# Optimization experiments

Measured on AMD Instinct MI355X. Metric: run time of the kernel, lower is better.

## Reference

```python
import jax, jax.numpy as jnp
import numpy as np

B, Q, D = 4, 1024, 1024
N, DH = 16, 64  # n_head, d_head
SCALE = 1.0 / DH ** 0.5
LN_EPS = 1e-5


def setup_inputs() -> dict:
    key = jax.random.key(0)
    ks = jax.random.split(key, 10)
    return {
        "w": jax.random.normal(ks[0], (B, Q, D), jnp.float32),
        "r_emb": jax.random.normal(ks[1], (Q, N, DH), jnp.float32),
        "r_w_bias": jax.random.normal(ks[2], (N, DH), jnp.float32),
        "r_bias": jax.random.normal(ks[3], (Q, N), jnp.float32),
        # projection weights stored [in, out]; torch Linear init std = 1/sqrt(d_head)
        "Wq": jax.random.normal(ks[4], (D, N * DH), jnp.float32) * SCALE,
        "Wk": jax.random.normal(ks[5], (D, N * DH), jnp.float32) * SCALE,
        "Wv": jax.random.normal(ks[6], (D, N * DH), jnp.float32) * SCALE,
        "Wo": jax.random.normal(ks[7], (N * DH, D), jnp.float32) * SCALE,
        "ln_gamma": jnp.ones((D,), jnp.float32),
        "ln_beta": jnp.zeros((D,), jnp.float32),
    }


def _rel_shift(x):
    # x: [b, i, j, n]; pad a zero column at the end of j then drop j=0
    # equivalent to shifting left by one along j with a trailing zero.
    return jnp.concatenate([x[:, :, 1:, :], jnp.zeros_like(x[:, :, :1, :])], axis=2)


def reference(w, r_emb, r_w_bias, r_bias, Wq, Wk, Wv, Wo, ln_gamma, ln_beta):
    b, qlen, d = w.shape
    klen = qlen  # mems=None
    n, dh = r_w_bias.shape

    q_h = (w @ Wq).reshape(b, qlen, n, dh)
    k_h = (w @ Wk).reshape(b, klen, n, dh)
    v_h = (w @ Wv).reshape(b, klen, n, dh)

    rw_q = q_h + r_w_bias[None, None]                      # [b,q,n,dh]
    AC = jnp.einsum('bind,bjnd->bijn', rw_q, k_h)          # [b,q,k,n]
    B_ = jnp.einsum('bind,jnd->bijn', q_h, r_emb)          # [b,q,k,n]
    BD = _rel_shift(B_ + r_bias[None, None])               # [b,q,k,n]

    attn_score = (AC + BD) * SCALE
    attn_prob = jax.nn.softmax(attn_score, axis=2)
    attn_vec = jnp.einsum('bijn,bjnd->bind', attn_prob, v_h)
    attn_out = attn_vec.reshape(b, qlen, n * dh) @ Wo

    out = w + attn_out  # residual (post-lnorm path)
    mu = jnp.mean(out, axis=-1, keepdims=True)
    var = jnp.var(out, axis=-1, keepdims=True)
    return (out - mu) / jnp.sqrt(var + LN_EPS) * ln_gamma + ln_beta
```

## Files before the change

### kernel.cpp

```cpp
#include <hip/hip_runtime.h>
#include <hip/hip_bf16.h>

using f16 = _Float16;
typedef _Float16 f16x8 __attribute__((ext_vector_type(8)));
typedef _Float16 f16x4 __attribute__((ext_vector_type(4)));
typedef float f32x4 __attribute__((ext_vector_type(4)));

#define AS1 __attribute__((address_space(1)))
#define AS3 __attribute__((address_space(3)))

constexpr int Bc = 4, Qc = 1024, Dc = 1024, Nh = 16, DHc = 64;
constexpr int BQ = Bc * Qc;
constexpr int NHEAD = Bc * Nh;
constexpr float ATT_SCALE = 0.125f;

__global__ void k_f2h(const float* __restrict__ src, f16* __restrict__ dst) {
    long i8 = ((long)blockIdx.x * blockDim.x + threadIdx.x) * 8;
    float4 a = *(const float4*)&src[i8];
    float4 b = *(const float4*)&src[i8 + 4];
    f16x8 o = { (f16)a.x, (f16)a.y, (f16)a.z, (f16)a.w,
                (f16)b.x, (f16)b.y, (f16)b.z, (f16)b.w };
    *(f16x8*)&dst[i8] = o;
}

struct Ptr4 { const float* p[4]; };
__global__ void k_transpose4(Ptr4 srcs, f16* __restrict__ dst) {
    __shared__ f16 tile[32][33];
    const float* src = srcs.p[blockIdx.z];
    f16* d = dst + (long)blockIdx.z * Dc * Dc;
    int c0 = blockIdx.x * 32, r0 = blockIdx.y * 32;
#pragma unroll
    for (int dy = 0; dy < 32; dy += 8) {
        int r = r0 + threadIdx.y + dy, c = c0 + threadIdx.x;
        tile[threadIdx.y + dy][threadIdx.x] = (f16)src[(long)r * Dc + c];
    }
    __syncthreads();
#pragma unroll
    for (int dy = 0; dy < 32; dy += 8) {
        int c = c0 + threadIdx.y + dy, r = r0 + threadIdx.x;
        d[(long)c * Dc + r] = tile[threadIdx.x][threadIdx.y + dy];
    }
}

__global__ void k_fill_remb(const float* __restrict__ remb, f16* __restrict__ Kt) {
    long gid = (long)blockIdx.x * blockDim.x + threadIdx.x;
    int d8 = (int)(gid & 7) * 8;
    int j = (int)((gid >> 3) & 1023);
    int h = (int)(gid >> 13);
    int n = h & 15;
    f16x8 kv;
    if (j < 1023) {
        const float* rp = &remb[((long)(j + 1) * 16 + n) * 64 + d8];
        float4 r0 = *(const float4*)rp, r1 = *(const float4*)(rp + 4);
        kv[0] = (f16)r0.x; kv[1] = (f16)r0.y; kv[2] = (f16)r0.z; kv[3] = (f16)r0.w;
        kv[4] = (f16)r1.x; kv[5] = (f16)r1.y; kv[6] = (f16)r1.z; kv[7] = (f16)r1.w;
    } else {
        kv = f16x8{};
    }
    *(f16x8*)&Kt[(((long)h << 10) + j) * 128 + 64 + d8] = kv;
}

template <int BM, int BN, int BK, int WROWS, int WCOLS, int EPI>
__global__ __launch_bounds__(256) void k_gemm_nt(
    const f16* __restrict__ A, const f16* __restrict__ Bt, void* __restrict__ Cv,
    const float* __restrict__ aux, f16* __restrict__ qtp, f16* __restrict__ ktp,
    f16* __restrict__ vtp, int lda, int ldb, int ldc, int K)
{
    constexpr int TM = BM / (WROWS * 16);
    constexpr int TN = BN / (WCOLS * 16);
    __shared__ __align__(16) f16 sA[BM * BK];
    __shared__ __align__(16) f16 sB[BN * BK];

    const int tid = threadIdx.x;
    const int lane = tid & 63, wave = tid >> 6;
    const int wm = wave / WCOLS, wn = wave % WCOLS;
    const int m0 = blockIdx.y * BM, n0 = blockIdx.x * BN;

    f32x4 acc[TM][TN] = {};

    const int lrow = lane & 15;
    const int kq = (lane >> 4) * 8;
    const int srow = lane >> 2;
    const int scol = (lane & 3) * 8;

    for (int k0 = 0; k0 < K; k0 += BK) {
        __syncthreads();
        constexpr int CHA = BM * BK / 512;
#pragma unroll
        for (int ch = 0; ch < CHA / 4; ++ch) {
            int cc = ch * 4 + wave;
            __builtin_amdgcn_global_load_lds(
                (const AS1 void*)(const void*)&A[(long)(m0 + cc * 16 + srow) * lda + k0 + scol],
                (AS3 void*)(void*)&sA[cc * 512], 16, 0, 0);
        }
        constexpr int CHB = BN * BK / 512;
#pragma unroll
        for (int ch = 0; ch < CHB / 4; ++ch) {
            int cc = ch * 4 + wave;
            __builtin_amdgcn_global_load_lds(
                (const AS1 void*)(const void*)&Bt[(long)(n0 + cc * 16 + srow) * ldb + k0 + scol],
                (AS3 void*)(void*)&sB[cc * 512], 16, 0, 0);
        }
        __syncthreads();

        f16x8 af[TM], bfr[TN];
#pragma unroll
        for (int mi = 0; mi < TM; ++mi)
            af[mi] = *(const f16x8*)&sA[(wm * TM * 16 + mi * 16 + lrow) * BK + kq];
#pragma unroll
        for (int ni = 0; ni < TN; ++ni)
            bfr[ni] = *(const f16x8*)&sB[(wn * TN * 16 + ni * 16 + lrow) * BK + kq];
#pragma unroll
        for (int mi = 0; mi < TM; ++mi)
#pragma unroll
            for (int ni = 0; ni < TN; ++ni)
                acc[mi][ni] = __builtin_amdgcn_mfma_f32_16x16x32_f16(af[mi], bfr[ni], acc[mi][ni], 0, 0, 0);
    }

    const int crow = (lane >> 4) * 4;
    const int ccol = lane & 15;
#pragma unroll
    for (int mi = 0; mi < TM; ++mi)
#pragma unroll
        for (int ni = 0; ni < TN; ++ni)
#pragma unroll
            for (int r = 0; r < 4; ++r) {
                int gm = m0 + wm * TM * 16 + mi * 16 + crow + r;
                int gn = n0 + wn * TN * 16 + ni * 16 + ccol;
                float val = acc[mi][ni][r];
                if constexpr (EPI == 0) {
                    ((f16*)Cv)[(long)gm * ldc + gn] = (f16)val;
                } else {
                    int seg = n0 >> 10;
                    int col = gn & 1023;
                    int n = col >> 6, d = col & 63, b = gm >> 10, i = gm & 1023;
                    long rowbase = ((((long)((b << 4) + n) << 10) + i) << 7);
                    if (seg == 0) {
                        qtp[rowbase + d] = (f16)(val + aux[col]);
                        qtp[rowbase + 64 + d] = (f16)val;
                    } else if (seg == 1) {
                        ktp[rowbase + d] = (f16)val;
                    } else {
                        vtp[(((long)(b << 10) + col) << 10) + i] = (f16)val;
                    }
                }
            }
}

__global__ __launch_bounds__(256, 2) void k_flash(
    const f16* __restrict__ Qt, const f16* __restrict__ Kt,
    const f16* __restrict__ vT, const float* __restrict__ r_bias,
    f16* __restrict__ avp)
{
    constexpr int LDL = 136;
    __shared__ __align__(16) f16 sK[128 * LDL];
    __shared__ __align__(16) f16 sV[64 * LDL];
    __shared__ float sRB[128];

    const int tid = threadIdx.x, lane = tid & 63, wave = tid >> 6;
    const int bid = blockIdx.x;
    const int h = (((bid >> 3) & 7) << 3) | (bid & 7);
    const int i0 = (bid >> 6) * 128;
    const int b = h >> 4, n = h & 15;

    const f16* Qh = Qt + (long)h * Qc * 128;
    const f16* Kh = Kt + (long)h * Qc * 128;
    const f16* Vh = vT + (long)h * DHc * Qc;

    const int lrow = lane & 15;
    const int quad = lane >> 4;
    const int kq = quad * 8;

    f16x8 aq[2][4];
#pragma unroll
    for (int t = 0; t < 2; ++t)
#pragma unroll
        for (int kc = 0; kc < 4; ++kc)
            aq[t][kc] = *(const f16x8*)&Qh[(long)(i0 + wave * 32 + t * 16 + lrow) * 128 + kc * 32 + kq];

    float m_i[2] = {-1e30f, -1e30f}, l_i[2] = {0.0f, 0.0f};
    f32x4 o_acc[2][4] = {};

    for (int j0 = 0; j0 < Qc; j0 += 128) {
        __syncthreads();
        for (int idx = tid; idx < 128 * 16; idx += 256) {
            int r = idx >> 4, c = (idx & 15) * 8;
            *(uint4*)&sK[r * LDL + c] = *(const uint4*)&Kh[(long)(j0 + r) * 128 + c];
        }
        for (int idx = tid; idx < 64 * 16; idx += 256) {
            int r = idx >> 4, c = (idx & 15) * 8;
            *(uint4*)&sV[r * LDL + c] = *(const uint4*)&Vh[(long)r * Qc + j0 + c];
        }
        if (tid < 128) {
            int j = j0 + tid;
            sRB[tid] = (j < Qc - 1) ? r_bias[(j + 1) * Nh + n] : 0.0f;
        }
        __syncthreads();

        f32x4 s_acc[2][8] = {};
#pragma unroll
        for (int kc = 0; kc < 4; ++kc)
#pragma unroll
            for (int ni = 0; ni < 8; ++ni) {
                f16x8 bk = *(const f16x8*)&sK[(ni * 16 + lrow) * LDL + kc * 32 + kq];
                s_acc[0][ni] = __builtin_amdgcn_mfma_f32_16x16x32_f16(bk, aq[0][kc], s_acc[0][ni], 0, 0, 0);
                s_acc[1][ni] = __builtin_amdgcn_mfma_f32_16x16x32_f16(bk, aq[1][kc], s_acc[1][ni], 0, 0, 0);
            }

        f16x4 pf[2][8];
        float alpha_t[2];
#pragma unroll
        for (int t = 0; t < 2; ++t) {
            float mx = -1e30f;
#pragma unroll
            for (int ni = 0; ni < 8; ++ni) {
                f32x4 rb4 = *(const f32x4*)&sRB[ni * 16 + quad * 4];
#pragma unroll
                for (int r = 0; r < 4; ++r) {
                    float v = (s_acc[t][ni][r] + rb4[r]) * ATT_SCALE;
                    s_acc[t][ni][r] = v;
                    mx = fmaxf(mx, v);
                }
            }
            mx = fmaxf(mx, __shfl_xor(mx, 16));
            mx = fmaxf(mx, __shfl_xor(mx, 32));
            float mn = fmaxf(m_i[t], mx);
            float alpha = __expf(m_i[t] - mn);
            float sm = 0.0f;
#pragma unroll
            for (int ni = 0; ni < 8; ++ni) {
                float e0 = __expf(s_acc[t][ni][0] - mn);
                float e1 = __expf(s_acc[t][ni][1] - mn);
                float e2 = __expf(s_acc[t][ni][2] - mn);
                float e3 = __expf(s_acc[t][ni][3] - mn);
                sm += (e0 + e1) + (e2 + e3);
                f16x4 pvv; pvv[0] = (f16)e0; pvv[1] = (f16)e1; pvv[2] = (f16)e2; pvv[3] = (f16)e3;
                pf[t][ni] = pvv;
            }
            sm += __shfl_xor(sm, 16);
            sm += __shfl_xor(sm, 32);
            l_i[t] = l_i[t] * alpha + sm;
            m_i[t] = mn;
            alpha_t[t] = alpha;
        }

#pragma unroll
        for (int t = 0; t < 2; ++t)
#pragma unroll
            for (int r = 0; r < 4; ++r) {
                float al = __shfl(alpha_t[t], quad * 4 + r);
#pragma unroll
                for (int dt = 0; dt < 4; ++dt) o_acc[t][dt][r] *= al;
            }

#pragma unroll
        for (int nj = 0; nj < 8; ++nj)
#pragma unroll
            for (int dt = 0; dt < 4; ++dt) {
                f16x4 bv = *(const f16x4*)&sV[(dt * 16 + lrow) * LDL + nj * 16 + quad * 4];
                o_acc[0][dt] = __builtin_amdgcn_mfma_f32_16x16x16f16(pf[0][nj], bv, o_acc[0][dt], 0, 0, 0);
                o_acc[1][dt] = __builtin_amdgcn_mfma_f32_16x16x16f16(pf[1][nj], bv, o_acc[1][dt], 0, 0, 0);
            }
    }

#pragma unroll
    for (int t = 0; t < 2; ++t) {
        float linv = 1.0f / l_i[t];
#pragma unroll
        for (int r = 0; r < 4; ++r) {
            float li = __shfl(linv, quad * 4 + r);
            int i = i0 + wave * 32 + t * 16 + quad * 4 + r;
#pragma unroll
            for (int dt = 0; dt < 4; ++dt) {
                int d = dt * 16 + lrow;
                avp[((long)(b * Qc + i) << 10) + n * 64 + d] = (f16)(o_acc[t][dt][r] * li);
            }
        }
    }
}

__global__ __launch_bounds__(256) void k_res_ln(const float* __restrict__ w, const f16* __restrict__ ao,
                                                const float* __restrict__ gamma, const float* __restrict__ beta,
                                                float* __restrict__ out) {
    const long base = (long)blockIdx.x * 1024;
    const int tid = threadIdx.x;
    float4 wv = *(const float4*)&w[base + tid * 4];
    f16x4 av = *(const f16x4*)&ao[base + tid * 4];
    float x[4] = { wv.x + (float)av[0], wv.y + (float)av[1],
                   wv.z + (float)av[2], wv.w + (float)av[3] };
    float s = x[0] + x[1] + x[2] + x[3];
    float s2 = x[0] * x[0] + x[1] * x[1] + x[2] * x[2] + x[3] * x[3];
#pragma unroll
    for (int off = 32; off; off >>= 1) { s += __shfl_down(s, off); s2 += __shfl_down(s2, off); }
    __shared__ float rs[4], rs2[4];
    if ((tid & 63) == 0) { rs[tid >> 6] = s; rs2[tid >> 6] = s2; }
    __syncthreads();
    s = rs[0] + rs[1] + rs[2] + rs[3];
    s2 = rs2[0] + rs2[1] + rs2[2] + rs2[3];
    float mu = s * (1.0f / 1024.0f);
    float var = s2 * (1.0f / 1024.0f) - mu * mu;
    float inv = rsqrtf(var + 1e-5f);
    float4 gv = *(const float4*)&gamma[tid * 4];
    float4 bv = *(const float4*)&beta[tid * 4];
    float4 o;
    o.x = (x[0] - mu) * inv * gv.x + bv.x;
    o.y = (x[1] - mu) * inv * gv.y + bv.y;
    o.z = (x[2] - mu) * inv * gv.z + bv.z;
    o.w = (x[3] - mu) * inv * gv.w + bv.w;
    *(float4*)&out[base + tid * 4] = o;
}

extern "C" void kernel_launch(void* const* d_in, const int* in_sizes, int n_in,
                              void* d_out, int out_size, void* d_ws, size_t ws_size,
                              hipStream_t stream) {
    const float* w_in   = (const float*)d_in[0];
    const float* r_emb  = (const float*)d_in[1];
    const float* r_wb   = (const float*)d_in[2];
    const float* r_bias = (const float*)d_in[3];
    const float* Wq     = (const float*)d_in[4];
    const float* Wk     = (const float*)d_in[5];
    const float* Wv     = (const float*)d_in[6];
    const float* Wo     = (const float*)d_in[7];
    const float* ln_g   = (const float*)d_in[8];
    const float* ln_b   = (const float*)d_in[9];
    float* out = (float*)d_out;

    char* p = (char*)d_ws;
    auto alloc = [&](size_t bytes) { char* r = p; p += (bytes + 255) & ~(size_t)255; return r; };
    f16* wh = (f16*)alloc((size_t)BQ * Dc * 2);
    f16* WT = (f16*)alloc((size_t)4 * Dc * Dc * 2);
    f16* Qt = (f16*)alloc((size_t)NHEAD * Qc * 128 * 2);
    f16* Kt = (f16*)alloc((size_t)NHEAD * Qc * 128 * 2);
    f16* vT = (f16*)alloc((size_t)BQ * Dc * 2);
    f16* WoT = WT + (size_t)3 * Dc * Dc;
    f16* avp = wh;
    f16* ao  = (f16*)Qt;

    k_f2h<<<(BQ * Dc) / (256 * 8), 256, 0, stream>>>(w_in, wh);

    Ptr4 srcs{{Wq, Wk, Wv, Wo}};
    k_transpose4<<<dim3(32, 32, 4), dim3(32, 8), 0, stream>>>(srcs, WT);

    k_fill_remb<<<(NHEAD * Qc * 8) / 256, 256, 0, stream>>>(r_emb, Kt);

    k_gemm_nt<128, 128, 32, 2, 2, 5><<<dim3(3 * Dc / 128, BQ / 128), 256, 0, stream>>>(
        wh, WT, nullptr, r_wb, Qt, Kt, vT, Dc, Dc, 0, Dc);

    k_flash<<<512, 256, 0, stream>>>(Qt, Kt, vT, r_bias, avp);

    k_gemm_nt<64, 128, 32, 2, 2, 0><<<dim3(Dc / 128, BQ / 64), 256, 0, stream>>>(
        avp, WoT, ao, nullptr, nullptr, nullptr, nullptr, Dc, Dc, Dc, Dc);

    k_res_ln<<<BQ, 256, 0, stream>>>(w_in, ao, ln_g, ln_b, out);
}
```

Measured before the change: 233.5 us.

## Store Q/K row-major and add r_w_bias inside flash kernel

The QKV GEMM epilogue now writes q and k as plain row-major [b*q, n*dh] f16 instead of a per-head 128-wide interleaved layout. The flash kernel builds its Q fragments itself, adding r_w_bias in registers and reusing q for the positional half. It also assembles each K tile in shared memory from kh and a separate compact r_emb buffer (Ke). This removes the duplicated Q write and the per-element bias load from the GEMM epilogue, and shrinks workspace. The cost is strided per-head loads in the flash kernel and the bias add now happening in f16 rather than in f32 before rounding.

New measurement: 223.8 us. -4.1%, faster.

```diff
diff --git a/kernel.cpp b/kernel.cpp
--- a/kernel.cpp
+++ b/kernel.cpp
@@ -42,7 +42,7 @@
     }
 }
 
-__global__ void k_fill_remb(const float* __restrict__ remb, f16* __restrict__ Kt) {
+__global__ void k_fill_remb(const float* __restrict__ remb, f16* __restrict__ Ke) {
     long gid = (long)blockIdx.x * blockDim.x + threadIdx.x;
     int d8 = (int)(gid & 7) * 8;
     int j = (int)((gid >> 3) & 1023);
@@ -57,14 +57,14 @@
     } else {
         kv = f16x8{};
     }
-    *(f16x8*)&Kt[(((long)h << 10) + j) * 128 + 64 + d8] = kv;
+    *(f16x8*)&Ke[(((long)h << 10) + j) * 64 + d8] = kv;
 }
 
 template <int BM, int BN, int BK, int WROWS, int WCOLS, int EPI>
 __global__ __launch_bounds__(256) void k_gemm_nt(
     const f16* __restrict__ A, const f16* __restrict__ Bt, void* __restrict__ Cv,
-    const float* __restrict__ aux, f16* __restrict__ qtp, f16* __restrict__ ktp,
-    f16* __restrict__ vtp, int lda, int ldb, int ldc, int K)
+    f16* __restrict__ qtp, f16* __restrict__ ktp, f16* __restrict__ vtp,
+    int lda, int ldb, int ldc, int K)
 {
     constexpr int TM = BM / (WROWS * 16);
     constexpr int TN = BN / (WCOLS * 16);
@@ -133,14 +133,12 @@
                 } else {
                     int seg = n0 >> 10;
                     int col = gn & 1023;
-                    int n = col >> 6, d = col & 63, b = gm >> 10, i = gm & 1023;
-                    long rowbase = ((((long)((b << 4) + n) << 10) + i) << 7);
                     if (seg == 0) {
-                        qtp[rowbase + d] = (f16)(val + aux[col]);
-                        qtp[rowbase + 64 + d] = (f16)val;
+                        qtp[(long)gm * 1024 + col] = (f16)val;
                     } else if (seg == 1) {
-                        ktp[rowbase + d] = (f16)val;
+                        ktp[(long)gm * 1024 + col] = (f16)val;
                     } else {
+                        int b = gm >> 10, i = gm & 1023;
                         vtp[(((long)(b << 10) + col) << 10) + i] = (f16)val;
                     }
                 }
@@ -148,8 +146,9 @@
 }
 
 __global__ __launch_bounds__(256, 2) void k_flash(
-    const f16* __restrict__ Qt, const f16* __restrict__ Kt,
-    const f16* __restrict__ vT, const float* __restrict__ r_bias,
+    const f16* __restrict__ qh, const f16* __restrict__ kh,
+    const f16* __restrict__ Ke, const f16* __restrict__ vT,
+    const float* __restrict__ rwb, const float* __restrict__ r_bias,
     f16* __restrict__ avp)
 {
     constexpr int LDL = 136;
@@ -163,29 +162,41 @@
     const int i0 = (bid >> 6) * 128;
     const int b = h >> 4, n = h & 15;
 
-    const f16* Qh = Qt + (long)h * Qc * 128;
-    const f16* Kh = Kt + (long)h * Qc * 128;
     const f16* Vh = vT + (long)h * DHc * Qc;
 
     const int lrow = lane & 15;
     const int quad = lane >> 4;
-    const int kq = quad * 8;
+
+    f16x8 rw0, rw1;
+#pragma unroll
+    for (int e = 0; e < 8; ++e) {
+        rw0[e] = (f16)rwb[n * 64 + quad * 8 + e];
+        rw1[e] = (f16)rwb[n * 64 + 32 + quad * 8 + e];
+    }
 
     f16x8 aq[2][4];
 #pragma unroll
-    for (int t = 0; t < 2; ++t)
-#pragma unroll
-        for (int kc = 0; kc < 4; ++kc)
-            aq[t][kc] = *(const f16x8*)&Qh[(long)(i0 + wave * 32 + t * 16 + lrow) * 128 + kc * 32 + kq];
+    for (int t = 0; t < 2; ++t) {
+        long rix = (long)(b * Qc + i0 + wave * 32 + t * 16 + lrow) * 1024 + n * 64;
+        f16x8 q0 = *(const f16x8*)&qh[rix + quad * 8];
+        f16x8 q1 = *(const f16x8*)&qh[rix + 32 + quad * 8];
+        aq[t][0] = q0 + rw0;
+        aq[t][1] = q1 + rw1;
+        aq[t][2] = q0;
+        aq[t][3] = q1;
+    }
 
     float m_i[2] = {-1e30f, -1e30f}, l_i[2] = {0.0f, 0.0f};
     f32x4 o_acc[2][4] = {};
 
     for (int j0 = 0; j0 < Qc; j0 += 128) {
         __syncthreads();
-        for (int idx = tid; idx < 128 * 16; idx += 256) {
-            int r = idx >> 4, c = (idx & 15) * 8;
-            *(uint4*)&sK[r * LDL + c] = *(const uint4*)&Kh[(long)(j0 + r) * 128 + c];
+        for (int idx = tid; idx < 1024; idx += 256) {
+            int r = idx >> 3, c = (idx & 7) * 8;
+            *(uint4*)&sK[r * LDL + c] =
+                *(const uint4*)&kh[(long)(b * Qc + j0 + r) * 1024 + n * 64 + c];
+            *(uint4*)&sK[r * LDL + 64 + c] =
+                *(const uint4*)&Ke[((long)h * Qc + j0 + r) * 64 + c];
         }
         for (int idx = tid; idx < 64 * 16; idx += 256) {
             int r = idx >> 4, c = (idx & 15) * 8;
@@ -202,7 +213,7 @@
         for (int kc = 0; kc < 4; ++kc)
 #pragma unroll
             for (int ni = 0; ni < 8; ++ni) {
-                f16x8 bk = *(const f16x8*)&sK[(ni * 16 + lrow) * LDL + kc * 32 + kq];
+                f16x8 bk = *(const f16x8*)&sK[(ni * 16 + lrow) * LDL + kc * 32 + quad * 8];
                 s_acc[0][ni] = __builtin_amdgcn_mfma_f32_16x16x32_f16(bk, aq[0][kc], s_acc[0][ni], 0, 0, 0);
                 s_acc[1][ni] = __builtin_amdgcn_mfma_f32_16x16x32_f16(bk, aq[1][kc], s_acc[1][ni], 0, 0, 0);
             }
@@ -329,27 +340,28 @@
     auto alloc = [&](size_t bytes) { char* r = p; p += (bytes + 255) & ~(size_t)255; return r; };
     f16* wh = (f16*)alloc((size_t)BQ * Dc * 2);
     f16* WT = (f16*)alloc((size_t)4 * Dc * Dc * 2);
-    f16* Qt = (f16*)alloc((size_t)NHEAD * Qc * 128 * 2);
-    f16* Kt = (f16*)alloc((size_t)NHEAD * Qc * 128 * 2);
+    f16* qh = (f16*)alloc((size_t)BQ * Dc * 2);
+    f16* kh = (f16*)alloc((size_t)BQ * Dc * 2);
+    f16* Ke = (f16*)alloc((size_t)NHEAD * Qc * DHc * 2);
     f16* vT = (f16*)alloc((size_t)BQ * Dc * 2);
     f16* WoT = WT + (size_t)3 * Dc * Dc;
     f16* avp = wh;
-    f16* ao  = (f16*)Qt;
+    f16* ao  = Ke;
 
     k_f2h<<<(BQ * Dc) / (256 * 8), 256, 0, stream>>>(w_in, wh);
 
     Ptr4 srcs{{Wq, Wk, Wv, Wo}};
     k_transpose4<<<dim3(32, 32, 4), dim3(32, 8), 0, stream>>>(srcs, WT);
 
-    k_fill_remb<<<(NHEAD * Qc * 8) / 256, 256, 0, stream>>>(r_emb, Kt);
+    k_fill_remb<<<(NHEAD * Qc * 8) / 256, 256, 0, stream>>>(r_emb, Ke);
 
     k_gemm_nt<128, 128, 32, 2, 2, 5><<<dim3(3 * Dc / 128, BQ / 128), 256, 0, stream>>>(
-        wh, WT, nullptr, r_wb, Qt, Kt, vT, Dc, Dc, 0, Dc);
-
-    k_flash<<<512, 256, 0, stream>>>(Qt, Kt, vT, r_bias, avp);
+        wh, WT, nullptr, qh, kh, vT, Dc, Dc, 0, Dc);
+
+    k_flash<<<512, 256, 0, stream>>>(qh, kh, Ke, vT, r_wb, r_bias, avp);
 
     k_gemm_nt<64, 128, 32, 2, 2, 0><<<dim3(Dc / 128, BQ / 64), 256, 0, stream>>>(
-        avp, WoT, ao, nullptr, nullptr, nullptr, nullptr, Dc, Dc, Dc, Dc);
+        avp, WoT, ao, nullptr, nullptr, nullptr, Dc, Dc, Dc, Dc);
 
     k_res_ln<<<BQ, 256, 0, stream>>>(w_in, ao, ln_g, ln_b, out);
 }
```
